# Performance work log

Measured on AMD Instinct MI355X. Metric: run time of the kernel, lower is better.

Reference implementation:

```python
import jax, jax.numpy as jnp
import numpy as np

N_PLACE = 100000
N_TRANS = 100000
E = 1000000
F_IN = 128
F_OUT = 64
H = 4
D = F_OUT // H
NEG_SLOPE = 0.2
EPS = 1e-16


def setup_inputs() -> dict:
    key = jax.random.key(0)
    ks = jax.random.split(key, 24)

    def rn(i, shape, s=1.0):
        return jax.random.normal(ks[i], shape, jnp.float32) * s

    def ei(i):
        k1, k2 = jax.random.split(ks[i])
        src = jax.random.randint(k1, (E,), 0, N_PLACE)
        dst = jax.random.randint(k2, (E,), 0, N_PLACE)
        return jnp.stack([src, dst]).astype(jnp.int32)

    return dict(
        x_place=rn(0, (N_PLACE, F_IN)),
        x_trans=rn(1, (N_TRANS, F_IN)),
        W_place=rn(2, (F_IN, F_OUT), 0.1),
        b_place=jnp.zeros((F_OUT,), jnp.float32),
        W_trans=rn(3, (F_IN, F_OUT), 0.1),
        b_trans=jnp.zeros((F_OUT,), jnp.float32),
        as_pt=rn(4, (H, D), 0.1), ad_pt=rn(5, (H, D), 0.1),
        as_tp=rn(6, (H, D), 0.1), ad_tp=rn(7, (H, D), 0.1),
        as_pp=rn(8, (H, D), 0.1), ad_pp=rn(9, (H, D), 0.1),
        as_tt=rn(10, (H, D), 0.1), ad_tt=rn(11, (H, D), 0.1),
        q=rn(12, (F_OUT,), 0.1),
        kW=rn(13, (F_OUT, F_OUT), 0.1),
        kb=jnp.zeros((F_OUT,), jnp.float32),
        ei_pt=ei(14), ei_tp=ei(15), ei_pp=ei(16), ei_tt=ei(17),
    )


def _rel(x_src, x_dst, ei, a_src, a_dst, n_dst):
    # Per-relation GAT-style attention (HANConv inner step).
    # x_src: [N_src, H, D], x_dst: [N_dst, H, D], ei: [2, E]
    src, dst = ei[0], ei[1]
    al_s = jnp.einsum('nhd,hd->nh', x_src, a_src)  # [N_src, H]
    al_d = jnp.einsum('nhd,hd->nh', x_dst, a_dst)  # [N_dst, H]
    alpha = jax.nn.leaky_relu(al_s[src] + al_d[dst], NEG_SLOPE)  # [E, H]
    # segment softmax over incoming edges of each dst node
    m = jax.ops.segment_max(alpha, dst, num_segments=n_dst)  # [N_dst, H]
    e = jnp.exp(alpha - m[dst])
    s = jax.ops.segment_sum(e, dst, num_segments=n_dst)
    a = e / (s[dst] + EPS)  # [E, H]
    out = jax.ops.segment_sum(x_src[src] * a[:, :, None], dst, num_segments=n_dst)
    return jax.nn.relu(out.reshape(n_dst, H * D))


def _group(outs, q, kW, kb):
    # HANConv semantic attention across relations targeting one node type.
    out = jnp.stack(outs)  # [R, N, F]
    score = jnp.einsum('f,rf->r', q, jnp.tanh(out @ kW + kb).mean(axis=1))  # [R]
    attn = jax.nn.softmax(score)
    return jnp.einsum('r,rnf->nf', attn, out)


def reference(x_place, x_trans, W_place, b_place, W_trans, b_trans,
              as_pt, ad_pt, as_tp, ad_tp, as_pp, ad_pp, as_tt, ad_tt,
              q, kW, kb, ei_pt, ei_tp, ei_pp, ei_tt):
    hp = (x_place @ W_place + b_place).reshape(N_PLACE, H, D)
    ht = (x_trans @ W_trans + b_trans).reshape(N_TRANS, H, D)
    out_t_pt = _rel(hp, ht, ei_pt, as_pt, ad_pt, N_TRANS)
    out_t_tt = _rel(ht, ht, ei_tt, as_tt, ad_tt, N_TRANS)
    out_p_tp = _rel(ht, hp, ei_tp, as_tp, ad_tp, N_PLACE)
    out_p_pp = _rel(hp, hp, ei_pp, as_pp, ad_pp, N_PLACE)
    out_place = _group([out_p_tp, out_p_pp], q, kW, kb)
    out_trans = _group([out_t_pt, out_t_tt], q, kW, kb)
    return out_place, out_trans
```

## Files before the change

### kernel.cpp

```cpp
#include <hip/hip_runtime.h>
#include <hip/hip_bf16.h>

#define NN 100000
#define NE 1000000
#define FI 128
#define FO 64
#define NB 196
#define CAP 8192
#define RELSTRIDE (256 * CAP)
#define TILE 4096
#define PROJ_BLOCKS 2048
#define PLACE_BLOCKS 128

typedef unsigned short u16;
typedef unsigned int u32;

__device__ __forceinline__ float bf2f(u16 u) {
    return __uint_as_float(((u32)u) << 16);
}
__device__ __forceinline__ u16 f2bf(float f) {
    __hip_bfloat16 h = __float2bfloat16(f);
    return *(u16*)&h;
}

__global__ __launch_bounds__(256) void init_kernel(int* __restrict__ bcursor,
                                                   float* __restrict__ mean_acc)
{
    const int rel = blockIdx.x;
    const int tid = threadIdx.x;
    bcursor[rel * 256 + tid] = tid * CAP;
    if (tid < 64) mean_acc[rel * 64 + tid] = 0.f;
}

__global__ __launch_bounds__(256) void phase1_kernel(
    const float* __restrict__ x_p, const float* __restrict__ W_p, const float* __restrict__ b_p,
    const float* __restrict__ p_a0, const float* __restrict__ p_a1,
    const float* __restrict__ p_a2, const float* __restrict__ p_a3,
    const float* __restrict__ x_t, const float* __restrict__ W_t, const float* __restrict__ b_t,
    const float* __restrict__ t_a0, const float* __restrict__ t_a1,
    const float* __restrict__ t_a2, const float* __restrict__ t_a3,
    u16* __restrict__ hb_place, u16* __restrict__ hb_trans,
    float* __restrict__ al_place, float* __restrict__ al_trans,
    const int* __restrict__ ei_pt, const int* __restrict__ ei_tt,
    const int* __restrict__ ei_tp, const int* __restrict__ ei_pp,
    int* __restrict__ bcursor, u32* __restrict__ packed)
{
    __shared__ float smem[FI * FO];
    const int bid = blockIdx.x;
    const int tid = threadIdx.x;

    if (bid < PROJ_BLOCKS) {
        const int ty = bid >> 10;
        const int bx = bid & 1023;
        const float* x = ty ? x_t : x_p;
        const float* W = ty ? W_t : W_p;
        const float* b = ty ? b_t : b_p;
        const float* a0 = ty ? t_a0 : p_a0;
        const float* a1 = ty ? t_a1 : p_a1;
        const float* a2 = ty ? t_a2 : p_a2;
        const float* a3 = ty ? t_a3 : p_a3;
        u16* hout = ty ? hb_trans : hb_place;
        float* al = ty ? al_trans : al_place;

        for (int i = tid; i < FI * FO; i += 256) smem[i] = W[i];
        __syncthreads();

        const int lane = tid & 63;
        const int wid  = tid >> 6;
        const int gw   = bx * 4 + wid;
        const int head = lane >> 4;

        const float bv  = b[lane];
        const float av0 = a0[lane];
        const float av1 = a1[lane];
        const float av2 = a2[lane];
        const float av3 = a3[lane];

        for (int n0 = gw * 4; n0 < NN; n0 += 4096 * 4) {
            const int m0 = __builtin_amdgcn_readfirstlane(n0);
            const float* __restrict__ xr0 = x + (size_t)m0 * FI;
            const float* __restrict__ xr1 = xr0 + FI;
            const float* __restrict__ xr2 = xr1 + FI;
            const float* __restrict__ xr3 = xr2 + FI;
            float c0 = bv, c1 = bv, c2 = bv, c3 = bv;
#pragma unroll
            for (int k = 0; k < FI; ++k) {
                const float w = smem[k * FO + lane];
                c0 = fmaf(xr0[k], w, c0);
                c1 = fmaf(xr1[k], w, c1);
                c2 = fmaf(xr2[k], w, c2);
                c3 = fmaf(xr3[k], w, c3);
            }
            hout[(size_t)m0 * FO + lane]       = f2bf(c0);
            hout[(size_t)(m0 + 1) * FO + lane] = f2bf(c1);
            hout[(size_t)(m0 + 2) * FO + lane] = f2bf(c2);
            hout[(size_t)(m0 + 3) * FO + lane] = f2bf(c3);

#pragma unroll
            for (int j = 0; j < 4; ++j) {
                const float acc = (j == 0) ? c0 : (j == 1) ? c1 : (j == 2) ? c2 : c3;
                float p0 = acc * av0, p1 = acc * av1, p2 = acc * av2, p3 = acc * av3;
#pragma unroll
                for (int off = 1; off < 16; off <<= 1) {
                    p0 += __shfl_xor(p0, off);
                    p1 += __shfl_xor(p1, off);
                    p2 += __shfl_xor(p2, off);
                    p3 += __shfl_xor(p3, off);
                }
                if ((lane & 15) == 0) {
                    const int nu = m0 + j;
                    al[0 * NN * 4 + nu * 4 + head] = p0;
                    al[1 * NN * 4 + nu * 4 + head] = p1;
                    al[2 * NN * 4 + nu * 4 + head] = p2;
                    al[3 * NN * 4 + nu * 4 + head] = p3;
                }
            }
        }
    } else {
        const int pb = bid - PROJ_BLOCKS;
        const int rel = pb >> 7;
        const int bx  = pb & 127;
        const int* ei = (rel == 0) ? ei_pt : (rel == 1) ? ei_tt : (rel == 2) ? ei_tp : ei_pp;
        u32* pk = packed + (size_t)rel * RELSTRIDE;

        int* lh = (int*)smem;
        int* lb = (int*)smem + 256;

        const int ntiles = (NE + TILE - 1) / TILE;
        for (int tile = bx; tile < ntiles; tile += PLACE_BLOCKS) {
            const int t0 = tile * TILE;
            lh[tid] = 0;
            __syncthreads();

            int d[TILE / 256];
#pragma unroll
            for (int i = 0; i < TILE / 256; ++i) {
                const int idx = t0 + i * 256 + tid;
                d[i] = (idx < NE) ? ei[NE + idx] : -1;
                if (d[i] >= 0) atomicAdd(&lh[d[i] >> 9], 1);
            }
            __syncthreads();
            if (lh[tid]) lb[tid] = atomicAdd(&bcursor[rel * 256 + tid], lh[tid]);
            __syncthreads();
#pragma unroll
            for (int i = 0; i < TILE / 256; ++i) {
                const int idx = t0 + i * 256 + tid;
                if (d[i] >= 0) {
                    const int src = ei[idx];
                    const int slot = atomicAdd(&lb[d[i] >> 9], 1);
                    pk[slot] = ((u32)(d[i] & 511) << 17) | (u32)src;
                }
            }
            __syncthreads();
        }
    }
}

__global__ __launch_bounds__(256) void csr_build(
    const u32* __restrict__ packed, const int* __restrict__ bcursor,
    int2* __restrict__ ofp, int* __restrict__ perm)
{
    const int rel = blockIdx.y;
    const int b = blockIdx.x;
    const int tid = threadIdx.x;
    const int base = b * CAP;
    const int cnt  = bcursor[rel * 256 + b] - base;
    const u32* pk = packed + (size_t)rel * RELSTRIDE + base;
    int2* of = ofp + (size_t)rel * NN;
    int* pm = perm + (size_t)rel * RELSTRIDE;

    __shared__ int h[512];
    __shared__ int cur[512];
    h[tid] = 0; h[tid + 256] = 0;
    __syncthreads();
    for (int i = tid; i < cnt; i += 256)
        atomicAdd(&h[pk[i] >> 17], 1);
    __syncthreads();
    const int o0 = h[tid], o1 = h[tid + 256];
    for (int off = 1; off < 512; off <<= 1) {
        const int a0 = (tid >= off) ? h[tid - off] : 0;
        const int a1 = (tid + 256 >= off) ? h[tid + 256 - off] : 0;
        __syncthreads();
        h[tid] += a0; h[tid + 256] += a1;
        __syncthreads();
    }
    const int e0 = base + h[tid] - o0;
    const int e1 = base + h[tid + 256] - o1;
    const int gd0 = b * 512 + tid;
    const int gd1 = gd0 + 256;
    if (gd0 < NN) of[gd0] = make_int2(e0, e0 + o0);
    if (gd1 < NN) of[gd1] = make_int2(e1, e1 + o1);
    cur[tid] = e0; cur[tid + 256] = e1;
    __syncthreads();
    for (int i = tid; i < cnt; i += 256) {
        const u32 e = pk[i];
        const int slot = atomicAdd(&cur[e >> 17], 1);
        pm[slot] = (int)(e & 0x1FFFFu);
    }
}

#define EDGE4(pm_, als_, hb_, cc, advh_, num_, den_, head_, lane_)                                  \
    {                                                                                               \
        const int s0 = pm_[cc], s1 = pm_[cc + 1], s2 = pm_[cc + 2], s3 = pm_[cc + 3];               \
        const float4 v0 = *(const float4*)(als_ + (size_t)s0 * 4);                                  \
        const float4 v1 = *(const float4*)(als_ + (size_t)s1 * 4);                                  \
        const float4 v2 = *(const float4*)(als_ + (size_t)s2 * 4);                                  \
        const float4 v3 = *(const float4*)(als_ + (size_t)s3 * 4);                                  \
        float a0 = ((head_ == 0) ? v0.x : (head_ == 1) ? v0.y : (head_ == 2) ? v0.z : v0.w) + advh_;\
        float a1 = ((head_ == 0) ? v1.x : (head_ == 1) ? v1.y : (head_ == 2) ? v1.z : v1.w) + advh_;\
        float a2 = ((head_ == 0) ? v2.x : (head_ == 1) ? v2.y : (head_ == 2) ? v2.z : v2.w) + advh_;\
        float a3 = ((head_ == 0) ? v3.x : (head_ == 1) ? v3.y : (head_ == 2) ? v3.z : v3.w) + advh_;\
        a0 = a0 > 0.f ? a0 : 0.2f * a0;                                                             \
        a1 = a1 > 0.f ? a1 : 0.2f * a1;                                                             \
        a2 = a2 > 0.f ? a2 : 0.2f * a2;                                                             \
        a3 = a3 > 0.f ? a3 : 0.2f * a3;                                                             \
        const float e0 = __expf(a0), e1 = __expf(a1), e2 = __expf(a2), e3 = __expf(a3);             \
        const float h0 = bf2f(hb_[(size_t)s0 * FO + lane_]);                                        \
        const float h1 = bf2f(hb_[(size_t)s1 * FO + lane_]);                                        \
        const float h2 = bf2f(hb_[(size_t)s2 * FO + lane_]);                                        \
        const float h3 = bf2f(hb_[(size_t)s3 * FO + lane_]);                                        \
        num_ = fmaf(h0, e0, num_);                                                                  \
        num_ = fmaf(h1, e1, num_);                                                                  \
        num_ = fmaf(h2, e2, num_);                                                                  \
        num_ = fmaf(h3, e3, num_);                                                                  \
        den_ += (e0 + e1) + (e2 + e3);                                                              \
    }

#define EDGE1(pm_, als_, hb_, cc, advh_, num_, den_, head_, lane_)                                  \
    {                                                                                               \
        const int s0 = pm_[cc];                                                                     \
        const float4 v0 = *(const float4*)(als_ + (size_t)s0 * 4);                                  \
        float a0 = ((head_ == 0) ? v0.x : (head_ == 1) ? v0.y : (head_ == 2) ? v0.z : v0.w) + advh_;\
        a0 = a0 > 0.f ? a0 : 0.2f * a0;                                                             \
        const float e0 = __expf(a0);                                                                \
        const float h0 = bf2f(hb_[(size_t)s0 * FO + lane_]);                                        \
        num_ = fmaf(h0, e0, num_);                                                                  \
        den_ += e0;                                                                                 \
    }

__global__ __launch_bounds__(256) void acc_kernel(
    const u16* __restrict__ hb_place, const u16* __restrict__ hb_trans,
    const float* __restrict__ al_place, const float* __restrict__ al_trans,
    const int2* __restrict__ ofp, const int* __restrict__ perm,
    u16* __restrict__ outb)
{
    const int rel = blockIdx.y;
    const u16* hb; const float* als; const float* ald;
    if (rel == 0)      { hb = hb_place; als = al_place + 0 * NN * 4; ald = al_trans + 2 * NN * 4; }
    else if (rel == 1) { hb = hb_trans; als = al_trans + 1 * NN * 4; ald = al_trans + 3 * NN * 4; }
    else if (rel == 2) { hb = hb_trans; als = al_trans + 0 * NN * 4; ald = al_place + 2 * NN * 4; }
    else               { hb = hb_place; als = al_place + 1 * NN * 4; ald = al_place + 3 * NN * 4; }
    const int2* of = ofp + (size_t)rel * NN;
    const int* pm = perm + (size_t)rel * RELSTRIDE;
    u16* ob = outb + (size_t)rel * NN * FO;

    const int lane = threadIdx.x & 63;
    const int wid  = threadIdx.x >> 6;
    const int head = lane >> 4;

    const int gw = blockIdx.x * 4 + wid;
    const int nw = gridDim.x * 4;
    for (int n = gw; n < NN; n += 2 * nw) {
        const int n2 = n + nw;
        const int nu = __builtin_amdgcn_readfirstlane(n);
        const int2 be = of[nu];
        int c1 = be.x;
        const int end1 = be.y;
        const float advh1 = ald[nu * 4 + head];
        float num1 = 0.f, den1 = 0.f;

        if (n2 < NN) {
            const int nu2 = __builtin_amdgcn_readfirstlane(n2);
            const int2 be2 = of[nu2];
            int c2 = be2.x;
            const int end2 = be2.y;
            const float advh2 = ald[nu2 * 4 + head];
            float num2 = 0.f, den2 = 0.f;

            while (c1 + 4 <= end1 && c2 + 4 <= end2) {
                EDGE4(pm, als, hb, c1, advh1, num1, den1, head, lane);
                EDGE4(pm, als, hb, c2, advh2, num2, den2, head, lane);
                c1 += 4; c2 += 4;
            }
            for (; c1 + 4 <= end1; c1 += 4) EDGE4(pm, als, hb, c1, advh1, num1, den1, head, lane);
            for (; c1 < end1; ++c1)         EDGE1(pm, als, hb, c1, advh1, num1, den1, head, lane);
            for (; c2 + 4 <= end2; c2 += 4) EDGE4(pm, als, hb, c2, advh2, num2, den2, head, lane);
            for (; c2 < end2; ++c2)         EDGE1(pm, als, hb, c2, advh2, num2, den2, head, lane);

            const float outv1 = fmaxf(num1 / (den1 + 1e-16f), 0.f);
            const float outv2 = fmaxf(num2 / (den2 + 1e-16f), 0.f);
            ob[(size_t)nu * FO + lane]  = f2bf(outv1);
            ob[(size_t)nu2 * FO + lane] = f2bf(outv2);
        } else {
            for (; c1 + 4 <= end1; c1 += 4) EDGE4(pm, als, hb, c1, advh1, num1, den1, head, lane);
            for (; c1 < end1; ++c1)         EDGE1(pm, als, hb, c1, advh1, num1, den1, head, lane);
            const float outv1 = fmaxf(num1 / (den1 + 1e-16f), 0.f);
            ob[(size_t)nu * FO + lane] = f2bf(outv1);
        }
    }
}

__global__ __launch_bounds__(256) void sem_kernel(
    const u16* __restrict__ outb, const float* __restrict__ kW, const float* __restrict__ kb,
    float* __restrict__ mean_acc)
{
    const int rel = blockIdx.y;
    const u16* ob = outb + (size_t)rel * NN * FO;
    const int QN = NN / 4;

    const int lane = threadIdx.x & 63;
    const int wid  = threadIdx.x >> 6;

    float kwc[FO];
#pragma unroll
    for (int k = 0; k < FO; ++k) kwc[k] = kW[k * FO + lane];
    const float kbv = kb[lane];

    float ts = 0.f;
    const int gw = blockIdx.x * 4 + wid;
    const int nw = gridDim.x * 4;
    for (int n = gw; n < QN; n += nw) {
        const int r0 = __builtin_amdgcn_readfirstlane(n);
        const int r1 = r0 + QN;
        const int r2 = r0 + 2 * QN;
        const int r3 = r0 + 3 * QN;
        const u32* w0 = (const u32*)(ob + (size_t)r0 * FO);
        const u32* w1 = (const u32*)(ob + (size_t)r1 * FO);
        const u32* w2 = (const u32*)(ob + (size_t)r2 * FO);
        const u32* w3 = (const u32*)(ob + (size_t)r3 * FO);
        float y0 = kbv, y1 = kbv, y2 = kbv, y3 = kbv;
#pragma unroll
        for (int i = 0; i < 32; ++i) {
            const u32 a = w0[i], b = w1[i], c = w2[i], d = w3[i];
            y0 = fmaf(__uint_as_float(a << 16),         kwc[2 * i],     y0);
            y0 = fmaf(__uint_as_float(a & 0xffff0000u), kwc[2 * i + 1], y0);
            y1 = fmaf(__uint_as_float(b << 16),         kwc[2 * i],     y1);
            y1 = fmaf(__uint_as_float(b & 0xffff0000u), kwc[2 * i + 1], y1);
            y2 = fmaf(__uint_as_float(c << 16),         kwc[2 * i],     y2);
            y2 = fmaf(__uint_as_float(c & 0xffff0000u), kwc[2 * i + 1], y2);
            y3 = fmaf(__uint_as_float(d << 16),         kwc[2 * i],     y3);
            y3 = fmaf(__uint_as_float(d & 0xffff0000u), kwc[2 * i + 1], y3);
        }
        ts += (tanhf(y0) + tanhf(y1)) + (tanhf(y2) + tanhf(y3));
    }

    __shared__ float red[4][64];
    red[wid][lane] = ts;
    __syncthreads();
    if (wid == 0) {
        const float sum = red[0][lane] + red[1][lane] + red[2][lane] + red[3][lane];
        unsafeAtomicAdd(&mean_acc[rel * 64 + lane], sum);
    }
}

__global__ __launch_bounds__(256) void combine_kernel(
    const u16* __restrict__ outb, const float* __restrict__ mean_acc,
    const float* __restrict__ q, float* __restrict__ out)
{
    const int lane = threadIdx.x & 63;
    const int type = blockIdx.y;
    const int r0i = (type == 0) ? 2 : 0;

    const float qv = q[lane];
    float s0 = qv * mean_acc[r0i * 64 + lane] * (1.0f / (float)NN);
    float s1 = qv * mean_acc[(r0i + 1) * 64 + lane] * (1.0f / (float)NN);
#pragma unroll
    for (int off = 1; off < 64; off <<= 1) {
        s0 += __shfl_xor(s0, off);
        s1 += __shfl_xor(s1, off);
    }
    const float m = fmaxf(s0, s1);
    const float e0 = expf(s0 - m), e1 = expf(s1 - m);
    const float a0 = e0 / (e0 + e1);
    const float a1 = e1 / (e0 + e1);

    const ushort4* o0 = (const ushort4*)(outb + (size_t)r0i * NN * FO);
    const ushort4* o1 = (const ushort4*)(outb + (size_t)(r0i + 1) * NN * FO);
    float4* dst = (float4*)(out + (size_t)type * NN * FO);
    const int n4 = NN * FO / 4;
    const int stride = gridDim.x * 256;
    for (int i = blockIdx.x * 256 + threadIdx.x; i < n4; i += stride) {
        const ushort4 u = o0[i];
        const ushort4 w = o1[i];
        float4 r;
        r.x = a0 * bf2f(u.x) + a1 * bf2f(w.x);
        r.y = a0 * bf2f(u.y) + a1 * bf2f(w.y);
        r.z = a0 * bf2f(u.z) + a1 * bf2f(w.z);
        r.w = a0 * bf2f(u.w) + a1 * bf2f(w.w);
        dst[i] = r;
    }
}

extern "C" void kernel_launch(void* const* d_in, const int* in_sizes, int n_in,
                              void* d_out, int out_size, void* d_ws, size_t ws_size,
                              hipStream_t stream)
{
    const float* x_place = (const float*)d_in[0];
    const float* x_trans = (const float*)d_in[1];
    const float* W_place = (const float*)d_in[2];
    const float* b_place = (const float*)d_in[3];
    const float* W_trans = (const float*)d_in[4];
    const float* b_trans = (const float*)d_in[5];
    const float* as_pt = (const float*)d_in[6];
    const float* ad_pt = (const float*)d_in[7];
    const float* as_tp = (const float*)d_in[8];
    const float* ad_tp = (const float*)d_in[9];
    const float* as_pp = (const float*)d_in[10];
    const float* ad_pp = (const float*)d_in[11];
    const float* as_tt = (const float*)d_in[12];
    const float* ad_tt = (const float*)d_in[13];
    const float* q  = (const float*)d_in[14];
    const float* kW = (const float*)d_in[15];
    const float* kb = (const float*)d_in[16];
    const int* ei_pt = (const int*)d_in[17];
    const int* ei_tp = (const int*)d_in[18];
    const int* ei_pp = (const int*)d_in[19];
    const int* ei_tt = (const int*)d_in[20];

    char* ws = (char*)d_ws;
    u16* hb_place = (u16*)ws;
    u16* hb_trans = hb_place + (size_t)NN * FO;
    float* al_place = (float*)(hb_trans + (size_t)NN * FO);
    float* al_trans = al_place + 4 * (size_t)NN * 4;
    u16* outb = (u16*)(al_trans + 4 * (size_t)NN * 4);
    int2* ofp = (int2*)(outb + 4 * (size_t)NN * FO);
    int* perm = (int*)(ofp + 4 * (size_t)NN);
    u32* packed = (u32*)(perm + 4 * (size_t)RELSTRIDE);
    int* bcursor = (int*)(packed + 4 * (size_t)RELSTRIDE);
    float* mean_acc = (float*)(bcursor + 4 * 256);

    init_kernel<<<4, 256, 0, stream>>>(bcursor, mean_acc);

    phase1_kernel<<<PROJ_BLOCKS + 4 * PLACE_BLOCKS, 256, 0, stream>>>(
        x_place, W_place, b_place, as_pt, as_pp, ad_tp, ad_pp,
        x_trans, W_trans, b_trans, as_tp, as_tt, ad_pt, ad_tt,
        hb_place, hb_trans, al_place, al_trans,
        ei_pt, ei_tt, ei_tp, ei_pp, bcursor, packed);

    csr_build<<<dim3(NB, 4), 256, 0, stream>>>(packed, bcursor, ofp, perm);

    acc_kernel<<<dim3(1024, 4), 256, 0, stream>>>(hb_place, hb_trans, al_place, al_trans,
                                                  ofp, perm, outb);

    sem_kernel<<<dim3(512, 4), 256, 0, stream>>>(outb, kW, kb, mean_acc);

    combine_kernel<<<dim3(1024, 2), 256, 0, stream>>>(outb, mean_acc, q, (float*)d_out);
}
```

Before: 503.1 us.

## Use bf16 MFMA for node projection and move attention logits into CSR kernel

```diff
diff --git a/kernel.cpp b/kernel.cpp
--- a/kernel.cpp
+++ b/kernel.cpp
@@ -9,11 +9,14 @@
 #define CAP 8192
 #define RELSTRIDE (256 * CAP)
 #define TILE 4096
-#define PROJ_BLOCKS 2048
+#define PROJ_T 512
 #define PLACE_BLOCKS 128
+#define ALB 128
 
 typedef unsigned short u16;
 typedef unsigned int u32;
+typedef __attribute__((ext_vector_type(8))) short short8t;
+typedef __attribute__((ext_vector_type(4))) float float4t;
 
 __device__ __forceinline__ float bf2f(u16 u) {
     return __uint_as_float(((u32)u) << 16);
@@ -34,97 +37,78 @@
 
 __global__ __launch_bounds__(256) void phase1_kernel(
     const float* __restrict__ x_p, const float* __restrict__ W_p, const float* __restrict__ b_p,
-    const float* __restrict__ p_a0, const float* __restrict__ p_a1,
-    const float* __restrict__ p_a2, const float* __restrict__ p_a3,
     const float* __restrict__ x_t, const float* __restrict__ W_t, const float* __restrict__ b_t,
-    const float* __restrict__ t_a0, const float* __restrict__ t_a1,
-    const float* __restrict__ t_a2, const float* __restrict__ t_a3,
     u16* __restrict__ hb_place, u16* __restrict__ hb_trans,
-    float* __restrict__ al_place, float* __restrict__ al_trans,
     const int* __restrict__ ei_pt, const int* __restrict__ ei_tt,
     const int* __restrict__ ei_tp, const int* __restrict__ ei_pp,
     int* __restrict__ bcursor, u32* __restrict__ packed)
 {
-    __shared__ float smem[FI * FO];
+    __shared__ int smem[512];
     const int bid = blockIdx.x;
     const int tid = threadIdx.x;
 
-    if (bid < PROJ_BLOCKS) {
-        const int ty = bid >> 10;
-        const int bx = bid & 1023;
-        const float* x = ty ? x_t : x_p;
-        const float* W = ty ? W_t : W_p;
-        const float* b = ty ? b_t : b_p;
-        const float* a0 = ty ? t_a0 : p_a0;
-        const float* a1 = ty ? t_a1 : p_a1;
-        const float* a2 = ty ? t_a2 : p_a2;
-        const float* a3 = ty ? t_a3 : p_a3;
-        u16* hout = ty ? hb_trans : hb_place;
-        float* al = ty ? al_trans : al_place;
-
-        for (int i = tid; i < FI * FO; i += 256) smem[i] = W[i];
-        __syncthreads();
+    if (bid < 2 * PROJ_T) {
+        const int ty = (bid >= PROJ_T);
+        const float* __restrict__ x = ty ? x_t : x_p;
+        const float* __restrict__ W = ty ? W_t : W_p;
+        const float* __restrict__ b = ty ? b_t : b_p;
+        u16* __restrict__ hout = ty ? hb_trans : hb_place;
 
         const int lane = tid & 63;
-        const int wid  = tid >> 6;
-        const int gw   = bx * 4 + wid;
-        const int head = lane >> 4;
-
-        const float bv  = b[lane];
-        const float av0 = a0[lane];
-        const float av1 = a1[lane];
-        const float av2 = a2[lane];
-        const float av3 = a3[lane];
-
-        for (int n0 = gw * 4; n0 < NN; n0 += 4096 * 4) {
-            const int m0 = __builtin_amdgcn_readfirstlane(n0);
-            const float* __restrict__ xr0 = x + (size_t)m0 * FI;
-            const float* __restrict__ xr1 = xr0 + FI;
-            const float* __restrict__ xr2 = xr1 + FI;
-            const float* __restrict__ xr3 = xr2 + FI;
-            float c0 = bv, c1 = bv, c2 = bv, c3 = bv;
-#pragma unroll
-            for (int k = 0; k < FI; ++k) {
-                const float w = smem[k * FO + lane];
-                c0 = fmaf(xr0[k], w, c0);
-                c1 = fmaf(xr1[k], w, c1);
-                c2 = fmaf(xr2[k], w, c2);
-                c3 = fmaf(xr3[k], w, c3);
-            }
-            hout[(size_t)m0 * FO + lane]       = f2bf(c0);
-            hout[(size_t)(m0 + 1) * FO + lane] = f2bf(c1);
-            hout[(size_t)(m0 + 2) * FO + lane] = f2bf(c2);
-            hout[(size_t)(m0 + 3) * FO + lane] = f2bf(c3);
-
-#pragma unroll
-            for (int j = 0; j < 4; ++j) {
-                const float acc = (j == 0) ? c0 : (j == 1) ? c1 : (j == 2) ? c2 : c3;
-                float p0 = acc * av0, p1 = acc * av1, p2 = acc * av2, p3 = acc * av3;
-#pragma unroll
-                for (int off = 1; off < 16; off <<= 1) {
-                    p0 += __shfl_xor(p0, off);
-                    p1 += __shfl_xor(p1, off);
-                    p2 += __shfl_xor(p2, off);
-                    p3 += __shfl_xor(p3, off);
-                }
-                if ((lane & 15) == 0) {
-                    const int nu = m0 + j;
-                    al[0 * NN * 4 + nu * 4 + head] = p0;
-                    al[1 * NN * 4 + nu * 4 + head] = p1;
-                    al[2 * NN * 4 + nu * 4 + head] = p2;
-                    al[3 * NN * 4 + nu * 4 + head] = p3;
-                }
-            }
+        const int wv   = tid >> 6;
+        const int g    = lane >> 4;
+        const int lo   = lane & 15;
+        const int wid  = ((bid & (PROJ_T - 1)) << 2) | wv;
+
+        short8t wf[4][4];
+#pragma unroll
+        for (int s = 0; s < 4; ++s)
+#pragma unroll
+            for (int t = 0; t < 4; ++t)
+#pragma unroll
+                for (int j = 0; j < 8; ++j)
+                    wf[s][t][j] = (short)f2bf(W[(s * 32 + g * 8 + j) * FO + t * 16 + lo]);
+
+        float bias[4];
+#pragma unroll
+        for (int t = 0; t < 4; ++t) bias[t] = b[t * 16 + lo];
+
+        for (int tile = wid; tile < NN / 16; tile += 2048) {
+            const int n0 = tile * 16;
+            float4t acc[4];
+#pragma unroll
+            for (int t = 0; t < 4; ++t) { acc[t][0] = 0.f; acc[t][1] = 0.f; acc[t][2] = 0.f; acc[t][3] = 0.f; }
+
+#pragma unroll
+            for (int s = 0; s < 4; ++s) {
+                const float* __restrict__ xr = x + (size_t)(n0 + lo) * FI + s * 32 + g * 8;
+                const float4 u = *(const float4*)xr;
+                const float4 v = *(const float4*)(xr + 4);
+                short8t af;
+                af[0] = (short)f2bf(u.x); af[1] = (short)f2bf(u.y);
+                af[2] = (short)f2bf(u.z); af[3] = (short)f2bf(u.w);
+                af[4] = (short)f2bf(v.x); af[5] = (short)f2bf(v.y);
+                af[6] = (short)f2bf(v.z); af[7] = (short)f2bf(v.w);
+#pragma unroll
+                for (int t = 0; t < 4; ++t)
+                    acc[t] = __builtin_amdgcn_mfma_f32_16x16x32_bf16(af, wf[s][t], acc[t], 0, 0, 0);
+            }
+
+#pragma unroll
+            for (int t = 0; t < 4; ++t)
+#pragma unroll
+                for (int j = 0; j < 4; ++j)
+                    hout[(size_t)(n0 + g * 4 + j) * FO + t * 16 + lo] = f2bf(acc[t][j] + bias[t]);
         }
     } else {
-        const int pb = bid - PROJ_BLOCKS;
+        const int pb = bid - 2 * PROJ_T;
         const int rel = pb >> 7;
         const int bx  = pb & 127;
         const int* ei = (rel == 0) ? ei_pt : (rel == 1) ? ei_tt : (rel == 2) ? ei_tp : ei_pp;
         u32* pk = packed + (size_t)rel * RELSTRIDE;
 
-        int* lh = (int*)smem;
-        int* lb = (int*)smem + 256;
+        int* lh = smem;
+        int* lb = smem + 256;
 
         const int ntiles = (NE + TILE - 1) / TILE;
         for (int tile = bx; tile < ntiles; tile += PLACE_BLOCKS) {
@@ -156,46 +140,95 @@
     }
 }
 
-__global__ __launch_bounds__(256) void csr_build(
+__global__ __launch_bounds__(256) void csr_build_al(
     const u32* __restrict__ packed, const int* __restrict__ bcursor,
-    int2* __restrict__ ofp, int* __restrict__ perm)
-{
-    const int rel = blockIdx.y;
-    const int b = blockIdx.x;
+    int2* __restrict__ ofp, int* __restrict__ perm,
+    const u16* __restrict__ hb_place, const u16* __restrict__ hb_trans,
+    const float* __restrict__ as_pt, const float* __restrict__ as_pp,
+    const float* __restrict__ ad_tp, const float* __restrict__ ad_pp,
+    const float* __restrict__ as_tp, const float* __restrict__ as_tt,
+    const float* __restrict__ ad_pt, const float* __restrict__ ad_tt,
+    float* __restrict__ al_place, float* __restrict__ al_trans)
+{
+    const int by = blockIdx.y;
+    const int bx = blockIdx.x;
     const int tid = threadIdx.x;
-    const int base = b * CAP;
-    const int cnt  = bcursor[rel * 256 + b] - base;
-    const u32* pk = packed + (size_t)rel * RELSTRIDE + base;
-    int2* of = ofp + (size_t)rel * NN;
-    int* pm = perm + (size_t)rel * RELSTRIDE;
-
-    __shared__ int h[512];
-    __shared__ int cur[512];
-    h[tid] = 0; h[tid + 256] = 0;
-    __syncthreads();
-    for (int i = tid; i < cnt; i += 256)
-        atomicAdd(&h[pk[i] >> 17], 1);
-    __syncthreads();
-    const int o0 = h[tid], o1 = h[tid + 256];
-    for (int off = 1; off < 512; off <<= 1) {
-        const int a0 = (tid >= off) ? h[tid - off] : 0;
-        const int a1 = (tid + 256 >= off) ? h[tid + 256 - off] : 0;
+
+    if (bx < NB) {
+        const int rel = by;
+        const int b = bx;
+        const int base = b * CAP;
+        const int cnt  = bcursor[rel * 256 + b] - base;
+        const u32* pk = packed + (size_t)rel * RELSTRIDE + base;
+        int2* of = ofp + (size_t)rel * NN;
+        int* pm = perm + (size_t)rel * RELSTRIDE;
+
+        __shared__ int h[512];
+        __shared__ int cur[512];
+        h[tid] = 0; h[tid + 256] = 0;
         __syncthreads();
-        h[tid] += a0; h[tid + 256] += a1;
+        for (int i = tid; i < cnt; i += 256)
+            atomicAdd(&h[pk[i] >> 17], 1);
         __syncthreads();
-    }
-    const int e0 = base + h[tid] - o0;
-    const int e1 = base + h[tid + 256] - o1;
-    const int gd0 = b * 512 + tid;
-    const int gd1 = gd0 + 256;
-    if (gd0 < NN) of[gd0] = make_int2(e0, e0 + o0);
-    if (gd1 < NN) of[gd1] = make_int2(e1, e1 + o1);
-    cur[tid] = e0; cur[tid + 256] = e1;
-    __syncthreads();
-    for (int i = tid; i < cnt; i += 256) {
-        const u32 e = pk[i];
-        const int slot = atomicAdd(&cur[e >> 17], 1);
-        pm[slot] = (int)(e & 0x1FFFFu);
+        const int o0 = h[tid], o1 = h[tid + 256];
+        for (int off = 1; off < 512; off <<= 1) {
+            const int a0 = (tid >= off) ? h[tid - off] : 0;
+            const int a1 = (tid + 256 >= off) ? h[tid + 256 - off] : 0;
+            __syncthreads();
+            h[tid] += a0; h[tid + 256] += a1;
+            __syncthreads();
+        }
+        const int e0 = base + h[tid] - o0;
+        const int e1 = base + h[tid + 256] - o1;
+        const int gd0 = b * 512 + tid;
+        const int gd1 = gd0 + 256;
+        if (gd0 < NN) of[gd0] = make_int2(e0, e0 + o0);
+        if (gd1 < NN) of[gd1] = make_int2(e1, e1 + o1);
+        cur[tid] = e0; cur[tid + 256] = e1;
+        __syncthreads();
+        for (int i = tid; i < cnt; i += 256) {
+            const u32 e = pk[i];
+            const int slot = atomicAdd(&cur[e >> 17], 1);
+            pm[slot] = (int)(e & 0x1FFFFu);
+        }
+    } else {
+        const int ab = bx - NB;
+        const int type = by >> 1;
+        const int part = by & 1;
+        const u16* hb = type ? hb_trans : hb_place;
+        float* al = type ? al_trans : al_place;
+        const float* a0 = type ? as_tp : as_pt;
+        const float* a1 = type ? as_tt : as_pp;
+        const float* a2 = type ? ad_pt : ad_tp;
+        const float* a3 = type ? ad_tt : ad_pp;
+
+        const int lane = tid & 63;
+        const int wv   = tid >> 6;
+        const int head = lane >> 4;
+        const float av0 = a0[lane];
+        const float av1 = a1[lane];
+        const float av2 = a2[lane];
+        const float av3 = a3[lane];
+
+        const int HN = NN / 2;
+        const int nw = ALB * 4;
+        for (int n = part * HN + ab * 4 + wv; n < (part + 1) * HN; n += nw) {
+            const float hv = bf2f(hb[(size_t)n * FO + lane]);
+            float p0 = hv * av0, p1 = hv * av1, p2 = hv * av2, p3 = hv * av3;
+#pragma unroll
+            for (int off = 1; off < 16; off <<= 1) {
+                p0 += __shfl_xor(p0, off);
+                p1 += __shfl_xor(p1, off);
+                p2 += __shfl_xor(p2, off);
+                p3 += __shfl_xor(p3, off);
+            }
+            if ((lane & 15) == 0) {
+                al[0 * NN * 4 + n * 4 + head] = p0;
+                al[1 * NN * 4 + n * 4 + head] = p1;
+                al[2 * NN * 4 + n * 4 + head] = p2;
+                al[3 * NN * 4 + n * 4 + head] = p3;
+            }
+        }
     }
 }
 
@@ -431,13 +464,18 @@
 
     init_kernel<<<4, 256, 0, stream>>>(bcursor, mean_acc);
 
-    phase1_kernel<<<PROJ_BLOCKS + 4 * PLACE_BLOCKS, 256, 0, stream>>>(
-        x_place, W_place, b_place, as_pt, as_pp, ad_tp, ad_pp,
-        x_trans, W_trans, b_trans, as_tp, as_tt, ad_pt, ad_tt,
-        hb_place, hb_trans, al_place, al_trans,
+    phase1_kernel<<<2 * PROJ_T + 4 * PLACE_BLOCKS, 256, 0, stream>>>(
+        x_place, W_place, b_place,
+        x_trans, W_trans, b_trans,
+        hb_place, hb_trans,
         ei_pt, ei_tt, ei_tp, ei_pp, bcursor, packed);
 
-    csr_build<<<dim3(NB, 4), 256, 0, stream>>>(packed, bcursor, ofp, perm);
+    csr_build_al<<<dim3(NB + ALB, 4), 256, 0, stream>>>(
+        packed, bcursor, ofp, perm,
+        hb_place, hb_trans,
+        as_pt, as_pp, ad_tp, ad_pp,
+        as_tp, as_tt, ad_pt, ad_tt,
+        al_place, al_trans);
 
     acc_kernel<<<dim3(1024, 4), 256, 0, stream>>>(hb_place, hb_trans, al_place, al_trans,
                                                   ofp, perm, outb);
```

Result: faster. 462.6 us (median of 2 runs) (-8.1%).
